# Optimization experiments

Measured on AMD Instinct MI355X. Metric: run time of the kernel, lower is better.

## Reference

```python
import jax, jax.numpy as jnp
import numpy as np

H, DM, LQ, LK, DK, DV = 16, 1024, 2048, 2048, 64, 64
B = 2

def setup_inputs() -> dict:
    key = jax.random.key(0)
    ks = jax.random.split(key, 12)
    s = 0.02  # init scale for weights
    return {
        "Q": jax.random.normal(ks[0], (B, LQ, DM), jnp.float32),
        "K": jax.random.normal(ks[1], (B, LK, DM), jnp.float32),
        "V": jax.random.normal(ks[2], (B, LK, DM), jnp.float32),
        "mask": jax.random.randint(ks[3], (B, LQ), 0, 2, jnp.int32),
        "W_Q": jax.random.normal(ks[4], (H * DK, DM), jnp.float32) * s,
        "b_Q": jnp.zeros((H * DK,), jnp.float32),
        "W_K": jax.random.normal(ks[5], (H * DK, DM), jnp.float32) * s,
        "b_K": jnp.zeros((H * DK,), jnp.float32),
        "W_V": jax.random.normal(ks[6], (H * DV, DM), jnp.float32) * s,
        "b_V": jnp.zeros((H * DV,), jnp.float32),
        "W_O": jax.random.normal(ks[7], (DM, H * DV), jnp.float32) * s,
        "b_O": jnp.zeros((DM,), jnp.float32),
    }

def reference(Q, K, V, mask, W_Q, b_Q, W_K, b_K, W_V, b_V, W_O, b_O):
    b = Q.shape[0]
    q = (Q @ W_Q.T + b_Q).reshape(b, LQ, H, DK)
    k = (K @ W_K.T + b_K).reshape(b, LK, H, DK)
    v = (V @ W_V.T + b_V).reshape(b, LK, H, DV)
    # scores: [b, h, q, k]
    A = jnp.einsum('bqhd,bkhd->bhqk', q, k) / jnp.sqrt(jnp.float32(DK))
    # mask masks whole QUERY rows; softmax is over the query axis (dim=1 in torch's [B*h, lq, lk])
    A = jnp.where(mask[:, None, :, None] == 0, -jnp.inf, A)
    alpha = jax.nn.softmax(A, axis=2)  # over query axis, per original masked branch
    out = jnp.einsum('bhqk,bkhd->bqhd', alpha, v).reshape(b, LQ, H * DV)
    return out @ W_O.T + b_O + Q  # output proj + residual
```

## Files before the change

kernel.cpp:

```cpp
#include <hip/hip_runtime.h>
#include <hip/hip_bf16.h>
#include <stdint.h>

using frag8 = __attribute__((ext_vector_type(8))) short;
using f32x4 = __attribute__((ext_vector_type(4))) float;

#define MFMA16 __builtin_amdgcn_mfma_f32_16x16x32_bf16

#if __has_builtin(__builtin_amdgcn_exp2f)
#define EXP2F(x) __builtin_amdgcn_exp2f(x)
#else
#define EXP2F(x) __expf((x) * 0.6931471805599453f)
#endif
#if __has_builtin(__builtin_amdgcn_rcpf)
#define RCPF(x) __builtin_amdgcn_rcpf(x)
#else
#define RCPF(x) (1.0f / (x))
#endif

#define SCALE_Q 0.18033688011112042f

__device__ __forceinline__ short f2bf(float f) {
    union { float f; uint32_t u; } x; x.f = f;
    uint32_t r = x.u + 0x7fffu + ((x.u >> 16) & 1u);
    return (short)(r >> 16);
}
__device__ __forceinline__ float bf2f(short s) {
    union { uint32_t u; float f; } x; x.u = ((uint32_t)(uint16_t)s) << 16;
    return x.f;
}
__device__ __forceinline__ uint32_t pack2bf(float a, float b) {
    float2 t; t.x = a; t.y = b;
    __hip_bfloat162 h = __float22bfloat162_rn(t);
    union { __hip_bfloat162 h; uint32_t u; } c; c.h = h;
    return c.u;
}

__global__ __launch_bounds__(256) void k_cvt_all(
    const float* __restrict__ s0, const float* __restrict__ s1,
    const float* __restrict__ s2, const float* __restrict__ s3,
    const float* __restrict__ s4, const float* __restrict__ s5,
    const float* __restrict__ s6,
    short* __restrict__ d0, short* __restrict__ d1, short* __restrict__ d2,
    short* __restrict__ d3, short* __restrict__ d4, short* __restrict__ d5,
    short* __restrict__ d6) {
    const int A4 = 1048576, W4 = 262144;
    int i = blockIdx.x * 256 + threadIdx.x;
    int st = gridDim.x * 256;
    const int total = 3 * A4 + 4 * W4;
    for (; i < total; i += st) {
        const float* s; short* d; int j;
        if (i < A4)            { s = s0; d = d0; j = i; }
        else if (i < 2 * A4)   { s = s1; d = d1; j = i - A4; }
        else if (i < 3 * A4)   { s = s2; d = d2; j = i - 2 * A4; }
        else {
            int t = i - 3 * A4; int seg = t / W4; j = t - seg * W4;
            s = seg == 0 ? s3 : seg == 1 ? s4 : seg == 2 ? s5 : s6;
            d = seg == 0 ? d3 : seg == 1 ? d4 : seg == 2 ? d5 : d6;
        }
        float4 v = reinterpret_cast<const float4*>(s)[j];
        ushort4 o;
        o.x = (uint16_t)f2bf(v.x); o.y = (uint16_t)f2bf(v.y);
        o.z = (uint16_t)f2bf(v.z); o.w = (uint16_t)f2bf(v.w);
        reinterpret_cast<ushort4*>(d)[j] = o;
    }
}

__device__ __forceinline__ void stage64x128(const short* __restrict__ g, int rs,
                                            short* lds, int tid) {
#pragma unroll
    for (int j = 0; j < 2; j++) {
        int chunk = j * 256 + tid;
        int row = chunk >> 3, c = chunk & 7;
        int sc = c ^ (row & 7);
        __builtin_amdgcn_global_load_lds(
            (const __attribute__((address_space(1))) uint32_t*)(g + (size_t)row * rs + sc * 8),
            (__attribute__((address_space(3))) uint32_t*)(lds + (j * 256 + (tid & 192)) * 8),
            16, 0, 0);
    }
}
__device__ __forceinline__ frag8 ldswz(const short* lds, int row, int cc) {
    return *(const frag8*)(lds + row * 64 + ((cc ^ (row & 7)) << 3));
}

__device__ __forceinline__ void stage_tiles(const short* __restrict__ As,
                                            const short* __restrict__ Bs,
                                            short* lA, short* lB,
                                            int w, int ln) {
#pragma unroll
    for (int j = 0; j < 2; j++) {
        int cb = (w * 2 + j) * 64;
        int c  = cb + ln;
        int row = c >> 2, c8 = c & 3;
        __builtin_amdgcn_global_load_lds(
            (const __attribute__((address_space(1))) uint32_t*)(As + row * 1024 + c8 * 8),
            (__attribute__((address_space(3))) uint32_t*)(lA + cb * 8), 16, 0, 0);
        __builtin_amdgcn_global_load_lds(
            (const __attribute__((address_space(1))) uint32_t*)(Bs + row * 1024 + c8 * 8),
            (__attribute__((address_space(3))) uint32_t*)(lB + cb * 8), 16, 0, 0);
    }
}

__global__ __launch_bounds__(256) void k_proj3(const short* __restrict__ A0,
                                               const short* __restrict__ A1,
                                               const short* __restrict__ A2,
                                               const short* __restrict__ B0,
                                               const short* __restrict__ B1,
                                               const short* __restrict__ B2,
                                               const float* __restrict__ bias0,
                                               const float* __restrict__ bias1,
                                               const float* __restrict__ bias2,
                                               short* __restrict__ dst0,
                                               short* __restrict__ dst1,
                                               short* __restrict__ dst2) {
    __shared__ short lA[2][4096];
    __shared__ short lB[2][4096];
    const int z = blockIdx.z;
    const short* A  = z == 0 ? A0 : z == 1 ? A1 : A2;
    const short* Bt = z == 0 ? B0 : z == 1 ? B1 : B2;
    const float* bias = z == 0 ? bias0 : z == 1 ? bias1 : bias2;
    short* dst = z == 0 ? dst0 : z == 1 ? dst1 : dst2;
    const float scale = z == 0 ? SCALE_Q : 1.0f;

    const int tid = threadIdx.x, w = tid >> 6, ln = tid & 63;
    const int wm = w >> 1, wn = w & 1, r16 = ln & 15, g = ln >> 4;
    const int tn = blockIdx.x * 128, tm = blockIdx.y * 128;
    const short* Ab = A + (size_t)tm * 1024;
    const short* Bb = Bt + (size_t)tn * 1024;

    f32x4 acc[4][4] = {};
    stage_tiles(Ab, Bb, &lA[0][0], &lB[0][0], w, ln);
    int buf = 0;
    for (int ks = 0; ks < 32; ks++) {
        __syncthreads();
        if (ks + 1 < 32)
            stage_tiles(Ab + (ks + 1) * 32, Bb + (ks + 1) * 32,
                        &lA[buf ^ 1][0], &lB[buf ^ 1][0], w, ln);
        frag8 af[4], bg[4];
#pragma unroll
        for (int mf = 0; mf < 4; mf++)
            af[mf] = *(const frag8*)&lA[buf][(wm * 64 + mf * 16 + r16) * 32 + g * 8];
#pragma unroll
        for (int nf = 0; nf < 4; nf++)
            bg[nf] = *(const frag8*)&lB[buf][(wn * 64 + nf * 16 + r16) * 32 + g * 8];
#pragma unroll
        for (int mf = 0; mf < 4; mf++)
#pragma unroll
            for (int nf = 0; nf < 4; nf++)
                acc[mf][nf] = MFMA16(af[mf], bg[nf], acc[mf][nf], 0, 0, 0);
        buf ^= 1;
    }
#pragma unroll
    for (int mf = 0; mf < 4; mf++)
#pragma unroll
        for (int nf = 0; nf < 4; nf++)
#pragma unroll
            for (int r = 0; r < 4; r++) {
                int m = tm + wm * 64 + mf * 16 + g * 4 + r;
                int n = tn + wn * 64 + nf * 16 + r16;
                float val = (acc[mf][nf][r] + bias[n]) * scale;
                int b = m >> 11, seq = m & 2047, h = n >> 6, d = n & 63;
                dst[((size_t)(b * 16 + h) * 2048 + seq) * 64 + d] = f2bf(val);
            }
}

__global__ __launch_bounds__(256, 4) void k_stats(const short* __restrict__ k_s,
                                                  const short* __restrict__ q_s,
                                                  const int* __restrict__ mask,
                                                  const short* __restrict__ v_s,
                                                  short* __restrict__ vhatT) {
    __shared__ short lQ[2][4096];
    __shared__ float lD[64];
    __shared__ short lT[64 * 70];
    const int wg = blockIdx.x;
    const int lin = (wg & 7) * 128 + (wg >> 3);
    const int bh = lin >> 5, kt = lin & 31;
    const int b = bh >> 4;
    const int tid = threadIdx.x, w = tid >> 6, ln = tid & 63;
    const int r16 = ln & 15, g = ln >> 4;
    const int kbase = kt * 64 + w * 16;

    const short* kp = k_s + ((size_t)bh * 2048 + kbase) * 64;
    frag8 kf[2];
#pragma unroll
    for (int kk = 0; kk < 2; kk++)
        kf[kk] = *(const frag8*)(kp + r16 * 64 + kk * 32 + g * 8);

    const short* qsp = q_s + (size_t)bh * 2048 * 64;
    float dacc[4] = {};
    const f32x4 z4 = {0.f, 0.f, 0.f, 0.f};

    stage64x128(qsp, 64, &lQ[0][0], tid);
    int buf = 0;
    for (int qb = 0; qb < 2048; qb += 64) {
        __syncthreads();
        if (qb + 64 < 2048)
            stage64x128(qsp + (size_t)(qb + 64) * 64, 64, &lQ[buf ^ 1][0], tid);
        const short* Qc = &lQ[buf][0];
#pragma unroll
        for (int nf = 0; nf < 4; nf++) {
            float fm = (float)mask[b * 2048 + qb + nf * 16 + r16];
            frag8 bq0 = ldswz(Qc, nf * 16 + r16, g);
            frag8 bq1 = ldswz(Qc, nf * 16 + r16, 4 + g);
            f32x4 s = MFMA16(kf[0], bq0, z4, 0, 0, 0);
            s = MFMA16(kf[1], bq1, s, 0, 0, 0);
#pragma unroll
            for (int r = 0; r < 4; r++)
                dacc[r] += fm * EXP2F(s[r]);
        }
        buf ^= 1;
    }
#pragma unroll
    for (int r = 0; r < 4; r++) {
        float v = dacc[r];
#pragma unroll
        for (int off = 1; off < 16; off <<= 1)
            v += __shfl_xor(v, off, 16);
        dacc[r] = v;
    }
    if (r16 == 0) {
#pragma unroll
        for (int r = 0; r < 4; r++)
            lD[w * 16 + g * 4 + r] = RCPF(dacc[r]);
    }
    const short* vrow = v_s + ((size_t)bh * 2048 + kt * 64) * 64;
#pragma unroll
    for (int i = 0; i < 4; i++) {
        int idx4 = i * 256 + tid;
        int row = idx4 >> 4, c4 = idx4 & 15;
        uint2 u = *(const uint2*)(vrow + (size_t)row * 64 + c4 * 4);
        *(uint32_t*)&lT[row * 70 + c4 * 4]     = u.x;
        *(uint32_t*)&lT[row * 70 + c4 * 4 + 2] = u.y;
    }
    __syncthreads();
    {
        int d = tid >> 2, kc = tid & 3;
        short* dstp = vhatT + ((size_t)bh * 64 + d) * 2048 + kt * 64 + kc * 16;
        uint32_t wd[8];
#pragma unroll
        for (int j2 = 0; j2 < 8; j2++) {
            int k0 = kc * 16 + j2 * 2;
            float v0 = bf2f(lT[k0 * 70 + d]) * lD[k0];
            float v1 = bf2f(lT[(k0 + 1) * 70 + d]) * lD[k0 + 1];
            wd[j2] = pack2bf(v0, v1);
        }
        uint4 o0 = {wd[0], wd[1], wd[2], wd[3]};
        uint4 o1 = {wd[4], wd[5], wd[6], wd[7]};
        *(uint4*)dstp = o0;
        *((uint4*)dstp + 1) = o1;
    }
}

__global__ __launch_bounds__(256, 4) void k_apply(const short* __restrict__ q_s,
                                                  const short* __restrict__ k_s,
                                                  const short* __restrict__ vhatT,
                                                  const int* __restrict__ mask,
                                                  short* __restrict__ attn) {
    __shared__ short lK[2][4096];
    __shared__ short lV[2][4096];
    __shared__ short lP[64 * 64];
    const int wg = blockIdx.x;
    const int lin = (wg & 7) * 128 + (wg >> 3);
    const int bh = lin >> 5, qt = lin & 31;
    const int b = bh >> 4, h = bh & 15;
    const int tid = threadIdx.x, w = tid >> 6, ln = tid & 63;
    const int r16 = ln & 15, g = ln >> 4;

    const short* qp = q_s + ((size_t)bh * 2048 + qt * 64 + w * 16) * 64;
    frag8 qf[2];
#pragma unroll
    for (int kk = 0; kk < 2; kk++)
        qf[kk] = *(const frag8*)(qp + r16 * 64 + kk * 32 + g * 8);

    const short* kp = k_s + (size_t)bh * 2048 * 64;
    const short* vp = vhatT + (size_t)bh * 64 * 2048;

    f32x4 oacc[4] = {};
    const f32x4 z4 = {0.f, 0.f, 0.f, 0.f};
    const int prow = w * 16 + r16, rx = prow & 7;

    stage64x128(kp, 64, &lK[0][0], tid);
    stage64x128(vp, 2048, &lV[0][0], tid);
    int buf = 0;
    for (int kb = 0; kb < 2048; kb += 64) {
        __syncthreads();
        if (kb + 64 < 2048) {
            stage64x128(kp + (size_t)(kb + 64) * 64, 64, &lK[buf ^ 1][0], tid);
            stage64x128(vp + kb + 64, 2048, &lV[buf ^ 1][0], tid);
        }
        const short* Kc = &lK[buf][0];
        const short* Vc = &lV[buf][0];
#pragma unroll
        for (int mf2 = 0; mf2 < 4; mf2++) {
            f32x4 s = z4;
#pragma unroll
            for (int kk = 0; kk < 2; kk++)
                s = MFMA16(ldswz(Kc, mf2 * 16 + r16, kk * 4 + g), qf[kk], s, 0, 0, 0);
            float e0 = EXP2F(s[0]), e1 = EXP2F(s[1]);
            float e2 = EXP2F(s[2]), e3 = EXP2F(s[3]);
            uint2 pk;
            pk.x = pack2bf(e0, e1);
            pk.y = pack2bf(e2, e3);
            int o = mf2 * 32 + g * 8;
            int addr = prow * 128 + (((o >> 4) ^ rx) << 4) + (o & 15);
            *(uint2*)((char*)lP + addr) = pk;
        }
        frag8 pa[2];
#pragma unroll
        for (int kk = 0; kk < 2; kk++)
            pa[kk] = *(const frag8*)((char*)lP + prow * 128 + (((kk * 4 + g) ^ rx) << 4));
#pragma unroll
        for (int nf = 0; nf < 4; nf++)
#pragma unroll
            for (int kk = 0; kk < 2; kk++)
                oacc[nf] = MFMA16(pa[kk], ldswz(Vc, nf * 16 + r16, kk * 4 + g), oacc[nf], 0, 0, 0);
        buf ^= 1;
    }
#pragma unroll
    for (int r = 0; r < 4; r++) {
        int q = qt * 64 + w * 16 + g * 4 + r;
        int mv = mask[b * 2048 + q];
#pragma unroll
        for (int nf = 0; nf < 4; nf++) {
            int d = nf * 16 + r16;
            float val = mv ? oacc[nf][r] : 0.f;
            attn[((size_t)(b * 2048 + q)) * 1024 + h * 64 + d] = f2bf(val);
        }
    }
}

__global__ __launch_bounds__(256) void k_final(const short* __restrict__ A,
                                               const short* __restrict__ Bt,
                                               const float* __restrict__ bias,
                                               const float* __restrict__ Qres,
                                               float* __restrict__ out) {
    __shared__ short lA[2][4096];
    __shared__ short lB[2][4096];
    const int tid = threadIdx.x, w = tid >> 6, ln = tid & 63;
    const int wm = w >> 1, wn = w & 1, r16 = ln & 15, g = ln >> 4;
    const int tn = blockIdx.x * 128, tm = blockIdx.y * 128;
    const short* Ab = A + (size_t)tm * 1024;
    const short* Bb = Bt + (size_t)tn * 1024;

    f32x4 acc[4][4] = {};
    stage_tiles(Ab, Bb, &lA[0][0], &lB[0][0], w, ln);
    int buf = 0;
    for (int ks = 0; ks < 32; ks++) {
        __syncthreads();
        if (ks + 1 < 32)
            stage_tiles(Ab + (ks + 1) * 32, Bb + (ks + 1) * 32,
                        &lA[buf ^ 1][0], &lB[buf ^ 1][0], w, ln);
        frag8 af[4], bg[4];
#pragma unroll
        for (int mf = 0; mf < 4; mf++)
            af[mf] = *(const frag8*)&lA[buf][(wm * 64 + mf * 16 + r16) * 32 + g * 8];
#pragma unroll
        for (int nf = 0; nf < 4; nf++)
            bg[nf] = *(const frag8*)&lB[buf][(wn * 64 + nf * 16 + r16) * 32 + g * 8];
#pragma unroll
        for (int mf = 0; mf < 4; mf++)
#pragma unroll
            for (int nf = 0; nf < 4; nf++)
                acc[mf][nf] = MFMA16(af[mf], bg[nf], acc[mf][nf], 0, 0, 0);
        buf ^= 1;
    }
#pragma unroll
    for (int mf = 0; mf < 4; mf++)
#pragma unroll
        for (int nf = 0; nf < 4; nf++)
#pragma unroll
            for (int r = 0; r < 4; r++) {
                int m = tm + wm * 64 + mf * 16 + g * 4 + r;
                int n = tn + wn * 64 + nf * 16 + r16;
                float val = acc[mf][nf][r] + bias[n] + Qres[(size_t)m * 1024 + n];
                out[(size_t)m * 1024 + n] = val;
            }
}

extern "C" void kernel_launch(void* const* d_in, const int* in_sizes, int n_in,
                              void* d_out, int out_size, void* d_ws, size_t ws_size,
                              hipStream_t stream) {
    (void)in_sizes; (void)n_in; (void)out_size; (void)ws_size;
    const float* Qf  = (const float*)d_in[0];
    const float* Kf  = (const float*)d_in[1];
    const float* Vf  = (const float*)d_in[2];
    const int*   msk = (const int*)d_in[3];
    const float* WQ  = (const float*)d_in[4];
    const float* bQ  = (const float*)d_in[5];
    const float* WK  = (const float*)d_in[6];
    const float* bK  = (const float*)d_in[7];
    const float* WV  = (const float*)d_in[8];
    const float* bV  = (const float*)d_in[9];
    const float* WO  = (const float*)d_in[10];
    const float* bO  = (const float*)d_in[11];
    float* out = (float*)d_out;

    char* p = (char*)d_ws;
    const size_t SZ_ACT = (size_t)4096 * 1024 * 2;
    const size_t SZ_W   = (size_t)1024 * 1024 * 2;
    short* Qb  = (short*)p; p += SZ_ACT;
    short* Kb  = (short*)p; p += SZ_ACT;
    short* Vb  = (short*)p; p += SZ_ACT;
    short* Wqb = (short*)p; p += SZ_W;
    short* Wkb = (short*)p; p += SZ_W;
    short* Wvb = (short*)p; p += SZ_W;
    short* Wob = (short*)p; p += SZ_W;
    short* q_s = (short*)p; p += SZ_ACT;
    short* k_s = (short*)p; p += SZ_ACT;
    short* v_s = (short*)p; p += SZ_ACT;
    short* vhatT = Kb;
    short* attn  = Qb;

    k_cvt_all<<<4096, 256, 0, stream>>>(Qf, Kf, Vf, WQ, WK, WV, WO,
                                        Qb, Kb, Vb, Wqb, Wkb, Wvb, Wob);

    k_proj3<<<dim3(8, 32, 3), 256, 0, stream>>>(Qb, Kb, Vb, Wqb, Wkb, Wvb,
                                                bQ, bK, bV, q_s, k_s, v_s);

    k_stats<<<1024, 256, 0, stream>>>(k_s, q_s, msk, v_s, vhatT);

    k_apply<<<1024, 256, 0, stream>>>(q_s, k_s, vhatT, msk, attn);

    k_final<<<dim3(8, 32), 256, 0, stream>>>(attn, Wob, bO, Qf, out);
}
```

Before: 173.6 us.

## Compact unmasked query rows to skip masked work in stats and apply

Adds a compaction kernel that builds per-batch lists of unmasked query indices, gathers the corresponding q rows into a dense buffer, and runs the softmax-denominator and apply kernels only over the compacted rows. Masked output rows are zero-filled by a separate kernel, and apply scatters results back to their original positions. This is meant to roughly halve the attention work for a random mask. The cost is three extra kernel launches, a gather pass and a full zeroing pass over the attention buffer.

```diff
diff --git a/kernel.cpp b/kernel.cpp
--- a/kernel.cpp
+++ b/kernel.cpp
@@ -34,6 +34,47 @@
     __hip_bfloat162 h = __float22bfloat162_rn(t);
     union { __hip_bfloat162 h; uint32_t u; } c; c.h = h;
     return c.u;
+}
+
+__global__ __launch_bounds__(64) void k_compact(const int* __restrict__ mask,
+                                                int* __restrict__ idx,
+                                                int* __restrict__ nU) {
+    const int b = blockIdx.x, ln = threadIdx.x;
+    const int* m = mask + b * 2048;
+    int* id = idx + b * 2048;
+    int base = 0;
+    for (int c = 0; c < 32; c++) {
+        int i = c * 64 + ln;
+        int mv = m[i];
+        unsigned long long bal = __ballot(mv != 0);
+        int rank = __popcll(bal & ((1ull << ln) - 1ull));
+        if (mv) id[base + rank] = i;
+        base += __popcll(bal);
+    }
+    if (ln == 0) nU[b] = base;
+    int nUr = (base + 63) & ~63;
+    for (int i = base + ln; i < nUr; i += 64) id[i] = 0;
+}
+
+__global__ __launch_bounds__(256) void k_zero(uint4* __restrict__ p, int n16) {
+    int i = blockIdx.x * 256 + threadIdx.x;
+    if (i < n16) { uint4 z = {0, 0, 0, 0}; p[i] = z; }
+}
+
+__global__ __launch_bounds__(256) void k_gather(const short* __restrict__ q_s,
+                                                const int* __restrict__ idx,
+                                                const int* __restrict__ nU,
+                                                short* __restrict__ q_c) {
+    const int bh = blockIdx.x, tile = blockIdx.y, b = bh >> 4;
+    const int n = nU[b], nUr = (n + 63) & ~63;
+    const int i = tile * 64 + (threadIdx.x >> 2);
+    if (i >= nUr) return;
+    const int src = idx[b * 2048 + i];
+    const uint4* sp = (const uint4*)(q_s + ((size_t)bh * 2048 + src) * 64);
+    uint4* dp = (uint4*)(q_c + ((size_t)bh * 2048 + i) * 64);
+    const int c = threadIdx.x & 3;
+    dp[c] = sp[c];
+    dp[c + 4] = sp[c + 4];
 }
 
 __global__ __launch_bounds__(256) void k_cvt_all(
@@ -165,8 +206,8 @@
 }
 
 __global__ __launch_bounds__(256, 4) void k_stats(const short* __restrict__ k_s,
-                                                  const short* __restrict__ q_s,
-                                                  const int* __restrict__ mask,
+                                                  const short* __restrict__ q_c,
+                                                  const int* __restrict__ nU,
                                                   const short* __restrict__ v_s,
                                                   short* __restrict__ vhatT) {
     __shared__ short lQ[2][4096];
@@ -176,6 +217,7 @@
     const int lin = (wg & 7) * 128 + (wg >> 3);
     const int bh = lin >> 5, kt = lin & 31;
     const int b = bh >> 4;
+    const int n = nU[b], nUr = (n + 63) & ~63;
     const int tid = threadIdx.x, w = tid >> 6, ln = tid & 63;
     const int r16 = ln & 15, g = ln >> 4;
     const int kbase = kt * 64 + w * 16;
@@ -186,29 +228,31 @@
     for (int kk = 0; kk < 2; kk++)
         kf[kk] = *(const frag8*)(kp + r16 * 64 + kk * 32 + g * 8);
 
-    const short* qsp = q_s + (size_t)bh * 2048 * 64;
+    const short* qsp = q_c + (size_t)bh * 2048 * 64;
     float dacc[4] = {};
     const f32x4 z4 = {0.f, 0.f, 0.f, 0.f};
 
-    stage64x128(qsp, 64, &lQ[0][0], tid);
-    int buf = 0;
-    for (int qb = 0; qb < 2048; qb += 64) {
-        __syncthreads();
-        if (qb + 64 < 2048)
-            stage64x128(qsp + (size_t)(qb + 64) * 64, 64, &lQ[buf ^ 1][0], tid);
-        const short* Qc = &lQ[buf][0];
-#pragma unroll
-        for (int nf = 0; nf < 4; nf++) {
-            float fm = (float)mask[b * 2048 + qb + nf * 16 + r16];
-            frag8 bq0 = ldswz(Qc, nf * 16 + r16, g);
-            frag8 bq1 = ldswz(Qc, nf * 16 + r16, 4 + g);
-            f32x4 s = MFMA16(kf[0], bq0, z4, 0, 0, 0);
-            s = MFMA16(kf[1], bq1, s, 0, 0, 0);
-#pragma unroll
-            for (int r = 0; r < 4; r++)
-                dacc[r] += fm * EXP2F(s[r]);
-        }
-        buf ^= 1;
+    if (nUr > 0) {
+        stage64x128(qsp, 64, &lQ[0][0], tid);
+        int buf = 0;
+        for (int qb = 0; qb < nUr; qb += 64) {
+            __syncthreads();
+            if (qb + 64 < nUr)
+                stage64x128(qsp + (size_t)(qb + 64) * 64, 64, &lQ[buf ^ 1][0], tid);
+            const short* Qc = &lQ[buf][0];
+#pragma unroll
+            for (int nf = 0; nf < 4; nf++) {
+                float fm = (qb + nf * 16 + r16 < n) ? 1.0f : 0.0f;
+                frag8 bq0 = ldswz(Qc, nf * 16 + r16, g);
+                frag8 bq1 = ldswz(Qc, nf * 16 + r16, 4 + g);
+                f32x4 s = MFMA16(kf[0], bq0, z4, 0, 0, 0);
+                s = MFMA16(kf[1], bq1, s, 0, 0, 0);
+#pragma unroll
+                for (int r = 0; r < 4; r++)
+                    dacc[r] += fm * EXP2F(s[r]);
+            }
+            buf ^= 1;
+        }
     }
 #pragma unroll
     for (int r = 0; r < 4; r++) {
@@ -251,10 +295,11 @@
     }
 }
 
-__global__ __launch_bounds__(256, 4) void k_apply(const short* __restrict__ q_s,
+__global__ __launch_bounds__(256, 4) void k_apply(const short* __restrict__ q_c,
                                                   const short* __restrict__ k_s,
                                                   const short* __restrict__ vhatT,
-                                                  const int* __restrict__ mask,
+                                                  const int* __restrict__ idx,
+                                                  const int* __restrict__ nU,
                                                   short* __restrict__ attn) {
     __shared__ short lK[2][4096];
     __shared__ short lV[2][4096];
@@ -263,10 +308,12 @@
     const int lin = (wg & 7) * 128 + (wg >> 3);
     const int bh = lin >> 5, qt = lin & 31;
     const int b = bh >> 4, h = bh & 15;
+    const int n = nU[b];
+    if (qt * 64 >= n) return;
     const int tid = threadIdx.x, w = tid >> 6, ln = tid & 63;
     const int r16 = ln & 15, g = ln >> 4;
 
-    const short* qp = q_s + ((size_t)bh * 2048 + qt * 64 + w * 16) * 64;
+    const short* qp = q_c + ((size_t)bh * 2048 + qt * 64 + w * 16) * 64;
     frag8 qf[2];
 #pragma unroll
     for (int kk = 0; kk < 2; kk++)
@@ -318,13 +365,14 @@
     }
 #pragma unroll
     for (int r = 0; r < 4; r++) {
-        int q = qt * 64 + w * 16 + g * 4 + r;
-        int mv = mask[b * 2048 + q];
-#pragma unroll
-        for (int nf = 0; nf < 4; nf++) {
-            int d = nf * 16 + r16;
-            float val = mv ? oacc[nf][r] : 0.f;
-            attn[((size_t)(b * 2048 + q)) * 1024 + h * 64 + d] = f2bf(val);
+        int lq = qt * 64 + w * 16 + g * 4 + r;
+        if (lq < n) {
+            int qg = idx[b * 2048 + lq];
+#pragma unroll
+            for (int nf = 0; nf < 4; nf++) {
+                int d = nf * 16 + r16;
+                attn[((size_t)(b * 2048 + qg)) * 1024 + h * 64 + d] = f2bf(oacc[nf][r]);
+            }
         }
     }
 }
@@ -408,8 +456,13 @@
     short* q_s = (short*)p; p += SZ_ACT;
     short* k_s = (short*)p; p += SZ_ACT;
     short* v_s = (short*)p; p += SZ_ACT;
+    int* idx = (int*)p; p += (size_t)2 * 2048 * 4;
+    int* nU  = (int*)p; p += 64;
     short* vhatT = Kb;
     short* attn  = Qb;
+    short* q_c   = Vb;
+
+    k_compact<<<2, 64, 0, stream>>>(msk, idx, nU);
 
     k_cvt_all<<<4096, 256, 0, stream>>>(Qf, Kf, Vf, WQ, WK, WV, WO,
                                         Qb, Kb, Vb, Wqb, Wkb, Wvb, Wob);
@@ -417,9 +470,13 @@
     k_proj3<<<dim3(8, 32, 3), 256, 0, stream>>>(Qb, Kb, Vb, Wqb, Wkb, Wvb,
                                                 bQ, bK, bV, q_s, k_s, v_s);
 
-    k_stats<<<1024, 256, 0, stream>>>(k_s, q_s, msk, v_s, vhatT);
-
-    k_apply<<<1024, 256, 0, stream>>>(q_s, k_s, vhatT, msk, attn);
+    k_gather<<<dim3(32, 32), 256, 0, stream>>>(q_s, idx, nU, q_c);
+
+    k_stats<<<1024, 256, 0, stream>>>(k_s, q_c, nU, v_s, vhatT);
+
+    k_zero<<<2048, 256, 0, stream>>>((uint4*)attn, 4096 * 1024 * 2 / 16);
+
+    k_apply<<<1024, 256, 0, stream>>>(q_c, k_s, vhatT, idx, nU, attn);
 
     k_final<<<dim3(8, 32), 256, 0, stream>>>(attn, Wob, bO, Qf, out);
 }
```

Measured after the change: 177.9 us. 2.5% more time.
